# Kernel optimization log

Measured on AMD Instinct MI355X. Metric: run time of the kernel, lower is better.

The kernel has to match this reference:

```python
import jax, jax.numpy as jnp
import numpy as np

# dims
B, P, H, W = 4, 512, 32, 32
C2 = P // 2            # 256 per-branch channels
HEAD = 4
DH = C2 // HEAD        # 64 head dim
L = H * W              # 1024 tokens
DI = 2 * C2            # 512 mamba d_inner (expand=2)
N = 64                 # d_state
R = (C2 + 15) // 16    # 16 dt_rank
KC = 4                 # d_conv


def setup_inputs() -> dict:
    key = jax.random.key(0)
    ks = jax.random.split(key, 32)
    f32 = jnp.float32
    def nrm(k, shape, s=0.02):
        return jax.random.normal(k, shape, f32) * s
    inp = {}
    inp['x'] = jax.random.normal(ks[0], (B, P, H, W), f32)
    # GambaCell rel-pos + gate conv
    inp['rel_h_c'] = jax.random.normal(ks[1], (1, C2, 1, H), f32)
    inp['rel_w_c'] = jax.random.normal(ks[2], (1, C2, W, 1), f32)
    inp['gate_w'] = nrm(ks[3], (C2, C2, 3))
    inp['gate_b'] = jnp.zeros((C2,), f32)
    # Mamba params
    inp['W_in'] = nrm(ks[4], (2 * DI, C2))
    inp['conv_w'] = nrm(ks[5], (DI, KC), 0.2)
    inp['conv_b'] = jnp.zeros((DI,), f32)
    inp['W_x'] = nrm(ks[6], (R + 2 * N, DI))
    inp['W_dt'] = nrm(ks[7], (DI, R), 0.1)
    inp['b_dt'] = jnp.full((DI,), -4.0, f32)
    inp['A_log'] = jnp.broadcast_to(jnp.log(jnp.arange(1, N + 1, dtype=f32)), (DI, N)).copy()
    inp['D_p'] = jnp.ones((DI,), f32)
    inp['W_out'] = nrm(ks[8], (C2, DI))
    # MHSA params (1x1 convs -> dense)
    inp['Wq'] = nrm(ks[9], (C2, C2)); inp['bq'] = jnp.zeros((C2,), f32)
    inp['Wk'] = nrm(ks[10], (C2, C2)); inp['bk'] = jnp.zeros((C2,), f32)
    inp['Wv'] = nrm(ks[11], (C2, C2)); inp['bv'] = jnp.zeros((C2,), f32)
    inp['rel_h_m'] = jax.random.normal(ks[12], (1, HEAD, DH, 1, H), f32) * 0.02
    inp['rel_w_m'] = jax.random.normal(ks[13], (1, HEAD, DH, W, 1), f32) * 0.02
    inp['reg_qk'] = jax.random.normal(ks[14], (1, L, L), f32)
    inp['reg_v'] = jax.random.normal(ks[15], (1, DH, L), f32)
    # Gating params
    inp['Wa'] = nrm(ks[16], (P, C2)); inp['ba'] = jnp.zeros((P,), f32)
    inp['Wb'] = nrm(ks[17], (P, C2)); inp['bb'] = jnp.zeros((P,), f32)
    inp['Wg'] = nrm(ks[18], (1, P)); inp['bg'] = jnp.zeros((1,), f32)
    return inp


def _silu(t):
    return t * jax.nn.sigmoid(t)


def _conv1x1(w, b, t):  # Conv2d kernel_size=1
    return jnp.einsum('oc,bchw->bohw', w, t) + b[None, :, None, None]


def _mamba(seq, W_in, conv_w, conv_b, W_x, W_dt, b_dt, A_log, D_p, W_out):
    # seq: (B, L, C2)
    Bn = seq.shape[0]
    xz = seq @ W_in.T                       # (B,L,2*DI)
    xi, z = jnp.split(xz, 2, axis=-1)
    # causal depthwise conv1d, kernel 4, left-pad 3, trimmed to L
    xc = jnp.transpose(xi, (0, 2, 1))       # (B,DI,L)
    xp = jnp.pad(xc, ((0, 0), (0, 0), (KC - 1, 0)))
    conv = conv_b[None, :, None]
    for kk in range(KC):
        conv = conv + conv_w[None, :, kk, None] * xp[:, :, kk:kk + L]
    xs = _silu(conv).transpose(0, 2, 1)     # (B,L,DI)
    x_dbl = xs @ W_x.T                      # (B,L,R+2N)
    dt = jax.nn.softplus(x_dbl[..., :R] @ W_dt.T + b_dt)   # (B,L,DI)
    Bm = x_dbl[..., R:R + N]                # (B,L,N)
    Cm = x_dbl[..., R + N:]                 # (B,L,N)
    A = -jnp.exp(A_log)                     # (DI,N)

    def step(h, t):
        dt_t, B_t, C_t, u_t = t             # (B,DI),(B,N),(B,N),(B,DI)
        dA = jnp.exp(dt_t[..., None] * A)   # (B,DI,N)
        h = dA * h + (dt_t * u_t)[..., None] * B_t[:, None, :]
        y = jnp.sum(h * C_t[:, None, :], axis=-1)
        return h, y

    h0 = jnp.zeros((Bn, DI, N), seq.dtype)
    scan_in = (dt.transpose(1, 0, 2), Bm.transpose(1, 0, 2),
               Cm.transpose(1, 0, 2), xs.transpose(1, 0, 2))
    _, ys = jax.lax.scan(step, h0, scan_in)  # (L,B,DI)
    y = ys.transpose(1, 0, 2) + D_p * xs
    y = y * _silu(z)
    return y @ W_out.T                      # (B,L,C2)


def _forward(x, rel_h_c, rel_w_c, gate_w, gate_b, W_in, conv_w, conv_b, W_x,
             W_dt, b_dt, A_log, D_p, W_out, Wq, bq, Wk, bk, Wv, bv,
             rel_h_m, rel_w_m, reg_qk, reg_v, Wa, ba, Wb, bb, Wg, bg):
    Bn = x.shape[0]
    x1, x2 = x[:, :C2], x[:, C2:]
    # --- GambaCell branch ---
    seq = x1.reshape(Bn, C2, L).transpose(0, 2, 1)          # (B,L,C2)
    pos = (rel_h_c + rel_w_c).reshape(1, C2, L).transpose(0, 2, 1)
    seq = seq + pos
    sc = seq.transpose(0, 2, 1)                             # (B,C2,L)
    ctx = jax.nn.sigmoid(
        jax.lax.conv_general_dilated(sc, gate_w, (1,), [(1, 1)],
                                     dimension_numbers=('NCH', 'OIH', 'NCH'))
        + gate_b[None, :, None]).transpose(0, 2, 1)          # (B,L,C2)
    ym = _mamba(seq, W_in, conv_w, conv_b, W_x, W_dt, b_dt, A_log, D_p, W_out)
    # faithful to original: view (B,L,C)->(B,C,H,W) with no permute
    out1 = (ym * ctx).reshape(Bn, C2, H, W)
    # --- MHSA branch ---
    q = _conv1x1(Wq, bq, x2).reshape(Bn, HEAD, DH, L)
    k = _conv1x1(Wk, bk, x2).reshape(Bn, HEAD, DH, L)
    v = _conv1x1(Wv, bv, x2).reshape(Bn, HEAD, DH, L)
    cc = jnp.einsum('bhdi,bhdj->bhij', q, k)                # content-content
    posm = (rel_h_m + rel_w_m).reshape(HEAD, DH, L)
    cp = jnp.einsum('hdi,bhdj->bhij', posm, q)              # position^T @ q
    energy = cc + cp                                         # (B,HEAD,L,L)
    e = jnp.concatenate([energy, jnp.broadcast_to(reg_qk[None], (Bn, 1, L, L))], axis=1)
    vp = jnp.concatenate([v, jnp.broadcast_to(reg_v[None], (Bn, 1, DH, L))], axis=1)
    attn = jax.nn.softmax(e, axis=-1)
    out = jnp.einsum('bndj,bnij->bndi', vp, attn)           # v @ attn^T
    out2 = out[:, :HEAD].reshape(Bn, C2, H, W)
    # --- Gating fusion ---
    a_proj = _conv1x1(Wa, ba, out1)
    b_proj = _conv1x1(Wb, bb, out2)
    ga = jax.nn.sigmoid(_conv1x1(Wg, bg, a_proj))
    gb = jax.nn.sigmoid(_conv1x1(Wg, bg, b_proj))
    return ga * a_proj + gb * b_proj                        # (B,P,H,W)


def reference(x, rel_h_c, rel_w_c, gate_w, gate_b, W_in, conv_w, conv_b, W_x,
              W_dt, b_dt, A_log, D_p, W_out, Wq, bq, Wk, bk, Wv, bv,
              rel_h_m, rel_w_m, reg_qk, reg_v, Wa, ba, Wb, bb, Wg, bg):
    return _forward(x, rel_h_c, rel_w_c, gate_w, gate_b, W_in, conv_w, conv_b,
                    W_x, W_dt, b_dt, A_log, D_p, W_out, Wq, bq, Wk, bk, Wv, bv,
                    rel_h_m, rel_w_m, reg_qk, reg_v, Wa, ba, Wb, bb, Wg, bg)
```

## Files before the change

kernel.cpp:

```cpp
#include <hip/hip_runtime.h>
#include <math.h>

static constexpr int Bn = 4, Pp = 512, C2 = 256, HEAD = 4, DHd = 64;
static constexpr int Ll = 1024, DIi = 512, Nn = 64, Rr = 16, KCc = 4;
static constexpr int XDW = 192;

#define DEVI __device__ __forceinline__

DEVI float sigf(float x){ return 1.0f/(1.0f+__expf(-x)); }
DEVI float softplusf(float x){ return x > 20.f ? x : log1pf(__expf(x)); }

DEVI unsigned short bfh(float f){
  unsigned int u = __float_as_uint(f);
  return (unsigned short)((u + 0x7FFFu + ((u>>16)&1u)) >> 16);
}
DEVI float bff(unsigned short h){ return __uint_as_float(((unsigned int)h)<<16); }
DEVI void wsplit(float v, unsigned short* __restrict__ h, unsigned short* __restrict__ l,
                 size_t i){
  unsigned short hh = bfh(v);
  h[i] = hh; l[i] = bfh(v - bff(hh));
}

typedef __attribute__((ext_vector_type(8))) short  bf8v;
typedef __attribute__((ext_vector_type(4))) float  f4v;
typedef __attribute__((ext_vector_type(8))) unsigned short u16x8;

__global__ void k_split(const float* __restrict__ src, unsigned short* __restrict__ h,
                        unsigned short* __restrict__ l, int n){
  int i = blockIdx.x*256 + threadIdx.x;
  if (i < n) wsplit(src[i], h, l, i);
}

__global__ void k_transpose(const float* __restrict__ x, const float* __restrict__ rh,
                            const float* __restrict__ rw, float* __restrict__ seq,
                            unsigned short* __restrict__ sh, unsigned short* __restrict__ sl,
                            unsigned short* __restrict__ x2h, unsigned short* __restrict__ x2l){
  __shared__ float t[32][33];
  int b = blockIdx.z, c0 = blockIdx.y*32, l0 = blockIdx.x*32;
  for (int i = threadIdx.y; i < 32; i += 8)
    t[i][threadIdx.x] = x[((size_t)(b*Pp + c0 + i)*Ll) + l0 + threadIdx.x];
  __syncthreads();
  for (int i = threadIdx.y; i < 32; i += 8){
    int l = l0 + i, c = c0 + threadIdx.x;
    float v = t[threadIdx.x][i];
    if (c < C2){
      float pos = rh[c*32 + (l & 31)] + rw[c*32 + (l >> 5)];
      float vv = v + pos;
      size_t o = (size_t)(b*Ll + l)*C2 + c;
      seq[o] = vv;
      wsplit(vv, sh, sl, o);
    } else {
      size_t o = (size_t)(b*Ll + l)*C2 + (c - C2);
      wsplit(v, x2h, x2l, o);
    }
  }
}

__global__ void __launch_bounds__(256) k_hgemm(
    const unsigned short* __restrict__ Ahp, const unsigned short* __restrict__ Alp,
    const unsigned short* __restrict__ Bhp, const unsigned short* __restrict__ Blp,
    float* __restrict__ C, const float* __restrict__ bias,
    int M, int N, int K, int lda, int ldb, int ldc,
    long sA1, long sA2, long sB1, long sB2, long sC1, long sC2, int act)
{
  __shared__ __align__(16) unsigned short Ah[64*40], Al[64*40], Bh[64*40], Bl[64*40];
  int z = blockIdx.z;
  const unsigned short* Abh = Ahp + (size_t)((z>>2)*sA1 + (z&3)*sA2);
  const unsigned short* Abl = Alp + (size_t)((z>>2)*sA1 + (z&3)*sA2);
  const unsigned short* Bbh = Bhp + (size_t)((z>>2)*sB1 + (z&3)*sB2);
  const unsigned short* Bbl = Blp + (size_t)((z>>2)*sB1 + (z&3)*sB2);
  float* Cb = C + (size_t)((z>>2)*sC1 + (z&3)*sC2);
  int m0 = blockIdx.y*64, n0 = blockIdx.x*64;
  int t = threadIdx.x;
  int w = t >> 6, l = t & 63;
  int g = l >> 4, r = l & 15;
  int row0 = w*16;

  f4v acc[4];
  #pragma unroll
  for (int j=0;j<4;++j) acc[j] = (f4v){0.f,0.f,0.f,0.f};

  int sr = t >> 2;
  int sc = (t & 3) * 8;

  for (int k0 = 0; k0 < K; k0 += 32){
    size_t ao = (size_t)(m0+sr)*lda + k0 + sc;
    size_t bo = (size_t)(n0+sr)*ldb + k0 + sc;
    *(u16x8*)&Ah[sr*40+sc] = *(const u16x8*)&Abh[ao];
    *(u16x8*)&Al[sr*40+sc] = *(const u16x8*)&Abl[ao];
    *(u16x8*)&Bh[sr*40+sc] = *(const u16x8*)&Bbh[bo];
    *(u16x8*)&Bl[sr*40+sc] = *(const u16x8*)&Bbl[bo];
    __syncthreads();
    bf8v a_h = *(const bf8v*)&Ah[(row0+r)*40 + g*8];
    bf8v a_l = *(const bf8v*)&Al[(row0+r)*40 + g*8];
    #pragma unroll
    for (int j=0;j<4;++j){
      bf8v b_h = *(const bf8v*)&Bh[(j*16+r)*40 + g*8];
      bf8v b_l = *(const bf8v*)&Bl[(j*16+r)*40 + g*8];
      acc[j] = __builtin_amdgcn_mfma_f32_16x16x32_bf16(a_h, b_h, acc[j], 0, 0, 0);
      acc[j] = __builtin_amdgcn_mfma_f32_16x16x32_bf16(a_h, b_l, acc[j], 0, 0, 0);
      acc[j] = __builtin_amdgcn_mfma_f32_16x16x32_bf16(a_l, b_h, acc[j], 0, 0, 0);
    }
    __syncthreads();
  }
  #pragma unroll
  for (int j=0;j<4;++j){
    int n = n0 + j*16 + r;
    float bv = bias ? bias[n] : 0.f;
    #pragma unroll
    for (int q=0;q<4;++q){
      int m = m0 + row0 + g*4 + q;
      float v = acc[j][q] + bv;
      if (act == 1) v = sigf(v);
      Cb[(size_t)m*ldc + n] = v;
    }
  }
}

__global__ void __launch_bounds__(256) k_h128(
    const unsigned short* __restrict__ Ahp, const unsigned short* __restrict__ Alp,
    const unsigned short* __restrict__ Bhp, const unsigned short* __restrict__ Blp,
    float* __restrict__ C, const float* __restrict__ bias,
    int M, int N, int K, int lda, int ldb, int ldc,
    long sA1, long sA2, long sB1, long sB2, long sC1, long sC2, int act)
{
  __shared__ __align__(16) unsigned short Ah[128*40], Al[128*40], Bh[128*40], Bl[128*40];
  int z = blockIdx.z;
  const unsigned short* Abh = Ahp + (size_t)((z>>2)*sA1 + (z&3)*sA2);
  const unsigned short* Abl = Alp + (size_t)((z>>2)*sA1 + (z&3)*sA2);
  const unsigned short* Bbh = Bhp + (size_t)((z>>2)*sB1 + (z&3)*sB2);
  const unsigned short* Bbl = Blp + (size_t)((z>>2)*sB1 + (z&3)*sB2);
  float* Cb = C + (size_t)((z>>2)*sC1 + (z&3)*sC2);
  int m0 = blockIdx.y*128, n0 = blockIdx.x*128;
  int t = threadIdx.x;
  int w = t >> 6, l = t & 63;
  int g = l >> 4, r = l & 15;
  int row0 = w*32;

  f4v acc[2][8];
  #pragma unroll
  for (int i=0;i<2;++i)
    #pragma unroll
    for (int j=0;j<8;++j) acc[i][j] = (f4v){0.f,0.f,0.f,0.f};

  int sr = t >> 1;
  int sc = (t & 1) * 16;

  for (int k0 = 0; k0 < K; k0 += 32){
    size_t ao = (size_t)(m0+sr)*lda + k0 + sc;
    size_t bo = (size_t)(n0+sr)*ldb + k0 + sc;
    *(u16x8*)&Ah[sr*40+sc]   = *(const u16x8*)&Abh[ao];
    *(u16x8*)&Ah[sr*40+sc+8] = *(const u16x8*)&Abh[ao+8];
    *(u16x8*)&Al[sr*40+sc]   = *(const u16x8*)&Abl[ao];
    *(u16x8*)&Al[sr*40+sc+8] = *(const u16x8*)&Abl[ao+8];
    *(u16x8*)&Bh[sr*40+sc]   = *(const u16x8*)&Bbh[bo];
    *(u16x8*)&Bh[sr*40+sc+8] = *(const u16x8*)&Bbh[bo+8];
    *(u16x8*)&Bl[sr*40+sc]   = *(const u16x8*)&Bbl[bo];
    *(u16x8*)&Bl[sr*40+sc+8] = *(const u16x8*)&Bbl[bo+8];
    __syncthreads();
    bf8v a_h0 = *(const bf8v*)&Ah[(row0+r)*40 + g*8];
    bf8v a_l0 = *(const bf8v*)&Al[(row0+r)*40 + g*8];
    bf8v a_h1 = *(const bf8v*)&Ah[(row0+16+r)*40 + g*8];
    bf8v a_l1 = *(const bf8v*)&Al[(row0+16+r)*40 + g*8];
    #pragma unroll
    for (int j=0;j<8;++j){
      bf8v b_h = *(const bf8v*)&Bh[(j*16+r)*40 + g*8];
      bf8v b_l = *(const bf8v*)&Bl[(j*16+r)*40 + g*8];
      acc[0][j] = __builtin_amdgcn_mfma_f32_16x16x32_bf16(a_h0, b_h, acc[0][j], 0, 0, 0);
      acc[0][j] = __builtin_amdgcn_mfma_f32_16x16x32_bf16(a_h0, b_l, acc[0][j], 0, 0, 0);
      acc[0][j] = __builtin_amdgcn_mfma_f32_16x16x32_bf16(a_l0, b_h, acc[0][j], 0, 0, 0);
      acc[1][j] = __builtin_amdgcn_mfma_f32_16x16x32_bf16(a_h1, b_h, acc[1][j], 0, 0, 0);
      acc[1][j] = __builtin_amdgcn_mfma_f32_16x16x32_bf16(a_h1, b_l, acc[1][j], 0, 0, 0);
      acc[1][j] = __builtin_amdgcn_mfma_f32_16x16x32_bf16(a_l1, b_h, acc[1][j], 0, 0, 0);
    }
    __syncthreads();
  }
  #pragma unroll
  for (int i=0;i<2;++i){
    #pragma unroll
    for (int j=0;j<8;++j){
      int n = n0 + j*16 + r;
      float bv = bias ? bias[n] : 0.f;
      #pragma unroll
      for (int q=0;q<4;++q){
        int m = m0 + row0 + i*16 + g*4 + q;
        float v = acc[i][j][q] + bv;
        if (act == 1) v = sigf(v);
        Cb[(size_t)m*ldc + n] = v;
      }
    }
  }
}

__global__ void k_padwx(const float* __restrict__ W_x, unsigned short* __restrict__ h,
                        unsigned short* __restrict__ l){
  int idx = blockIdx.x*256 + threadIdx.x;
  int row = idx >> 9;
  float v = (row < 144) ? W_x[(size_t)row*512 + (idx & 511)] : 0.f;
  wsplit(v, h, l, idx);
}

__global__ void k_im2col(const float* __restrict__ seq, unsigned short* __restrict__ h,
                         unsigned short* __restrict__ l){
  int idx = blockIdx.x*256 + threadIdx.x;
  int j  = idx % 768;
  int bl = idx / 768;
  int kk = j >> 8, c = j & 255;
  int ll = bl & 1023, b = bl >> 10;
  int ls = ll + kk - 1;
  float v = 0.f;
  if (ls >= 0 && ls < Ll) v = seq[(size_t)(b*Ll + ls)*C2 + c];
  wsplit(v, h, l, idx);
}

__global__ void k_packw(const float* __restrict__ gw, unsigned short* __restrict__ h,
                        unsigned short* __restrict__ l){
  int idx = blockIdx.x*256 + threadIdx.x;
  int j = idx % 768, o = idx / 768;
  int kk = j >> 8, i = j & 255;
  wsplit(gw[(size_t)(o*256 + i)*3 + kk], h, l, idx);
}

__global__ void k_dwconv(const float* __restrict__ xz, const float* __restrict__ cw,
                         const float* __restrict__ cb, float* __restrict__ xs,
                         unsigned short* __restrict__ h, unsigned short* __restrict__ l){
  int idx = blockIdx.x*256 + threadIdx.x;
  int d = idx & 511; int bl = idx >> 9; int ll = bl & 1023; int b = bl >> 10;
  float s = cb[d];
  #pragma unroll
  for (int kk = 0; kk < 4; ++kk){
    int ls = ll - 3 + kk;
    if (ls >= 0) s = fmaf(cw[d*4+kk], xz[(size_t)(b*Ll+ls)*1024 + d], s);
  }
  float v = s * sigf(s);
  xs[idx] = v;
  wsplit(v, h, l, idx);
}

__global__ void k_pret(const float* __restrict__ xdbl, const float* __restrict__ xs,
                       const float* __restrict__ W_dt, const float* __restrict__ b_dt,
                       float* __restrict__ dtT, float* __restrict__ dtuT){
  __shared__ float X[32][17];
  __shared__ float Wd[32][17];
  __shared__ float xsb[32][33];
  int b = blockIdx.z, d0 = blockIdx.y*32, l0 = blockIdx.x*32;
  int tx = threadIdx.x, ty = threadIdx.y;
  for (int i = ty; i < 32; i += 8){
    if (tx < 16)      X[i][tx]      = xdbl[(size_t)(b*Ll + l0 + i)*XDW + tx];
    else              Wd[i][tx-16]  = W_dt[(size_t)(d0 + i)*16 + tx - 16];
    xsb[i][tx] = xs[(size_t)(b*Ll + l0 + i)*512 + d0 + tx];
  }
  __syncthreads();
  for (int dy = ty; dy < 32; dy += 8){
    int d = d0 + dy;
    float v = b_dt[d];
    #pragma unroll
    for (int r = 0; r < 16; ++r) v = fmaf(Wd[dy][r], X[tx][r], v);
    float dt = softplusf(v);
    size_t o = ((size_t)(b*512 + d))*Ll + l0 + tx;
    dtT[o]  = dt;
    dtuT[o] = dt * xsb[tx][dy];
  }
}

__global__ void __launch_bounds__(256, 1) k_scan6(
    const float* __restrict__ dtT, const float* __restrict__ dtuT,
    const float* __restrict__ xdbl, const float* __restrict__ A_log,
    float* __restrict__ yT){
  __shared__ float Bs[32*64];
  __shared__ float Cs[32*64];
  __shared__ float pb[4*32*65];
  int t = threadIdx.x;
  int w = t >> 6, lane = t & 63;
  int blk = blockIdx.x;
  int b = blk >> 7, grp = blk & 127;
  int d = grp*4 + w;
  float Ac = -__expf(A_log[d*64 + lane]);
  float h = 0.f;
  size_t base = (size_t)b*Ll;
  size_t bd   = ((size_t)(b*512 + d))*Ll;
  int jl = lane & 31;
  bool lo = lane < 32;
  float* pbw = &pb[w*2080];
  for (int c0 = 0; c0 < Ll; c0 += 32){
    float dtv = 0.f, duv = 0.f;
    if (lo){
      dtv = dtT[bd + c0 + lane];
      duv = dtuT[bd + c0 + lane];
    }
    #pragma unroll
    for (int kk = 0; kk < 8; ++kk){
      int i = t + kk*256;
      int row = i >> 6, col = i & 63;
      size_t r2 = (base + c0 + row)*XDW;
      Bs[i] = xdbl[r2 + 16 + col];
      Cs[i] = xdbl[r2 + 80 + col];
    }
    __syncthreads();
    float ev[32], gv[32];
    #pragma unroll
    for (int l = 0; l < 32; ++l){
      float sdt = __shfl(dtv, l);
      float sdu = __shfl(duv, l);
      ev[l] = __expf(sdt*Ac);
      gv[l] = sdu*Bs[l*64 + lane];
    }
    #pragma unroll
    for (int l = 0; l < 32; ++l){
      h = fmaf(ev[l], h, gv[l]);
      pbw[l*65 + lane] = h*Cs[l*64 + lane];
    }
    __syncthreads();
    {
      const float* rp = &pbw[jl*65 + (lo ? 0 : 32)];
      float s0=0.f, s1=0.f, s2=0.f, s3=0.f;
      #pragma unroll
      for (int n = 0; n < 32; n += 4){
        s0 += rp[n]; s1 += rp[n+1]; s2 += rp[n+2]; s3 += rp[n+3];
      }
      float p = (s0+s1)+(s2+s3);
      p += __shfl_xor(p, 32);
      if (lo) yT[bd + c0 + jl] = p;
    }
    __syncthreads();
  }
}

__global__ void k_ytrans(const float* __restrict__ yT, const float* __restrict__ xs,
                         const float* __restrict__ xz, const float* __restrict__ D_p,
                         unsigned short* __restrict__ h, unsigned short* __restrict__ l){
  __shared__ float t[32][33];
  int b = blockIdx.z, d0 = blockIdx.y*32, l0 = blockIdx.x*32;
  int tx = threadIdx.x, ty = threadIdx.y;
  for (int i = ty; i < 32; i += 8)
    t[i][tx] = yT[((size_t)(b*512 + d0 + i))*Ll + l0 + tx];
  __syncthreads();
  for (int i = ty; i < 32; i += 8){
    int d = d0 + tx;
    size_t bl = (size_t)b*Ll + l0 + i;
    float p  = t[tx][i];
    float u  = xs[bl*512 + d];
    float zv = xz[bl*1024 + 512 + d];
    float v = (p + D_p[d]*u) * (zv * sigf(zv));
    wsplit(v, h, l, bl*512 + d);
  }
}

__global__ void k_pack_ab(const float* __restrict__ qt, const float* __restrict__ kt,
                          const float* __restrict__ rhm, const float* __restrict__ rwm,
                          unsigned short* __restrict__ Ahp, unsigned short* __restrict__ Alp,
                          unsigned short* __restrict__ Bhp, unsigned short* __restrict__ Blp){
  int idx = blockIdx.x*256 + threadIdx.x;
  int dd = idx & 127;
  int i  = (idx >> 7) & 1023;
  int h  = (idx >> 17) & 3;
  int b  = idx >> 19;
  float av, bv;
  if (dd < 64){
    size_t q = (size_t)(b*Ll + i)*C2 + h*64 + dd;
    av = qt[q]; bv = kt[q];
  } else {
    int d = dd - 64;
    av = rhm[(h*64+d)*32 + (i & 31)] + rwm[(h*64+d)*32 + (i >> 5)];
    bv = qt[(size_t)(b*Ll + i)*C2 + h*64 + d];
  }
  wsplit(av, Ahp, Alp, idx);
  wsplit(bv, Bhp, Blp, idx);
}

__global__ void k_vtrans(const float* __restrict__ vt, unsigned short* __restrict__ h,
                         unsigned short* __restrict__ l){
  __shared__ float t[32][33];
  int b = blockIdx.z, c0 = blockIdx.y*32, j0 = blockIdx.x*32;
  for (int i = threadIdx.y; i < 32; i += 8)
    t[i][threadIdx.x] = vt[(size_t)(b*Ll + j0 + i)*C2 + c0 + threadIdx.x];
  __syncthreads();
  for (int i = threadIdx.y; i < 32; i += 8){
    size_t o = ((size_t)(b*C2 + c0 + i))*Ll + j0 + threadIdx.x;
    wsplit(t[threadIdx.x][i], h, l, o);
  }
}

__global__ void __launch_bounds__(256) k_softmax(float* __restrict__ e){
  __shared__ float red[4];
  __shared__ float red2[4];
  size_t row = blockIdx.x;
  float* p = e + row*1024;
  int t = threadIdx.x;
  float v0 = p[t], v1 = p[t+256], v2 = p[t+512], v3 = p[t+768];
  float mx = fmaxf(fmaxf(v0,v1), fmaxf(v2,v3));
  #pragma unroll
  for (int off=32; off; off>>=1) mx = fmaxf(mx, __shfl_xor(mx, off));
  if ((t&63)==0) red[t>>6] = mx;
  __syncthreads();
  mx = fmaxf(fmaxf(red[0],red[1]), fmaxf(red[2],red[3]));
  v0 = __expf(v0-mx); v1 = __expf(v1-mx); v2 = __expf(v2-mx); v3 = __expf(v3-mx);
  float s = v0+v1+v2+v3;
  #pragma unroll
  for (int off=32; off; off>>=1) s += __shfl_xor(s, off);
  if ((t&63)==0) red2[t>>6] = s;
  __syncthreads();
  s = red2[0]+red2[1]+red2[2]+red2[3];
  float inv = 1.0f/s;
  unsigned short* ph = (unsigned short*)p;
  float r0 = v0*inv, r1 = v1*inv, r2 = v2*inv, r3 = v3*inv;
  unsigned short h0 = bfh(r0), h1 = bfh(r1), h2 = bfh(r2), h3 = bfh(r3);
  ph[t]      = h0; ph[1024+t]      = bfh(r0 - bff(h0));
  ph[t+256]  = h1; ph[1024+t+256]  = bfh(r1 - bff(h1));
  ph[t+512]  = h2; ph[1024+t+512]  = bfh(r2 - bff(h2));
  ph[t+768]  = h3; ph[1024+t+768]  = bfh(r3 - bff(h3));
}

__global__ void k_mulshuf(const float* __restrict__ ym, const float* __restrict__ ctx,
                          unsigned short* __restrict__ h, unsigned short* __restrict__ l){
  __shared__ float t[32][33];
  int b = blockIdx.z >> 2, s1 = blockIdx.z & 3;
  int c0 = blockIdx.y*32, s00 = blockIdx.x*32;
  for (int i = threadIdx.y; i < 32; i += 8){
    int c = c0 + i;
    int ll = c*4 + s1;
    size_t off = ((size_t)(b*Ll + ll))*C2 + s00 + threadIdx.x;
    t[i][threadIdx.x] = ym[off] * ctx[off];
  }
  __syncthreads();
  for (int i = threadIdx.y; i < 32; i += 8){
    int s0 = s00 + i, c = c0 + threadIdx.x;
    int s = s1*256 + s0;
    wsplit(t[threadIdx.x][i], h, l, ((size_t)(b*Ll + s))*C2 + c);
  }
}

__global__ void __launch_bounds__(256) k_gates(
    const float* __restrict__ ap, const float* __restrict__ bp,
    const float* __restrict__ Wg, const float* __restrict__ bg, float* __restrict__ g){
  __shared__ float ra[4], rb[4];
  int bl = blockIdx.x; int t = threadIdx.x;
  float sa = 0.f, sb = 0.f;
  const float* a = ap + (size_t)bl*512;
  const float* bq = bp + (size_t)bl*512;
  for (int pp = t; pp < 512; pp += 256){ float w = Wg[pp]; sa = fmaf(w, a[pp], sa); sb = fmaf(w, bq[pp], sb); }
  #pragma unroll
  for (int off=32; off; off>>=1){ sa += __shfl_xor(sa,off); sb += __shfl_xor(sb,off); }
  if ((t&63)==0){ ra[t>>6]=sa; rb[t>>6]=sb; }
  __syncthreads();
  if (t==0){
    float b0 = bg[0];
    g[bl]        = sigf(ra[0]+ra[1]+ra[2]+ra[3] + b0);
    g[4096 + bl] = sigf(rb[0]+rb[1]+rb[2]+rb[3] + b0);
  }
}

__global__ void k_final(const float* __restrict__ ap, const float* __restrict__ bp,
                        const float* __restrict__ g, float* __restrict__ out){
  int bpid = blockIdx.x; int b = bpid >> 9, p = bpid & 511;
  for (int l = threadIdx.x; l < Ll; l += 256){
    int bl = b*Ll + l;
    float ga = g[bl], gb = g[4096 + bl];
    out[((size_t)(b*Pp + p) << 10) + l] =
        ga*ap[(size_t)bl*512 + p] + gb*bp[(size_t)bl*512 + p];
  }
}

typedef unsigned short us;
static inline void hgemm(hipStream_t s, const us* Ah, const us* Al, const us* Bh, const us* Bl,
                         float* C, const float* bias, int M, int N, int K,
                         int lda, int ldb, int ldc, int act){
  dim3 g(N/64, M/64, 1), blk(256);
  k_hgemm<<<g, blk, 0, s>>>(Ah,Al,Bh,Bl,C,bias,M,N,K,lda,ldb,ldc, 0,0,0,0,0,0, act);
}

extern "C" void kernel_launch(void* const* d_in, const int* in_sizes, int n_in,
                              void* d_out, int out_size, void* d_ws, size_t ws_size,
                              hipStream_t stream) {
  const float* x      = (const float*)d_in[0];
  const float* rh_c   = (const float*)d_in[1];
  const float* rw_c   = (const float*)d_in[2];
  const float* gate_w = (const float*)d_in[3];
  const float* gate_b = (const float*)d_in[4];
  const float* W_in   = (const float*)d_in[5];
  const float* conv_w = (const float*)d_in[6];
  const float* conv_b = (const float*)d_in[7];
  const float* W_x    = (const float*)d_in[8];
  const float* W_dt   = (const float*)d_in[9];
  const float* b_dt   = (const float*)d_in[10];
  const float* A_log  = (const float*)d_in[11];
  const float* D_p    = (const float*)d_in[12];
  const float* W_out  = (const float*)d_in[13];
  const float* Wq     = (const float*)d_in[14];
  const float* bq     = (const float*)d_in[15];
  const float* Wk     = (const float*)d_in[16];
  const float* bk     = (const float*)d_in[17];
  const float* Wv     = (const float*)d_in[18];
  const float* bv     = (const float*)d_in[19];
  const float* rhm    = (const float*)d_in[20];
  const float* rwm    = (const float*)d_in[21];
  const float* Wa     = (const float*)d_in[24];
  const float* ba     = (const float*)d_in[25];
  const float* Wb     = (const float*)d_in[26];
  const float* bb     = (const float*)d_in[27];
  const float* Wg     = (const float*)d_in[28];
  const float* bg     = (const float*)d_in[29];
  float* out = (float*)d_out;
  float* ws  = (float*)d_ws;

  float* seq    = ws;
  float* x2seq  = ws +  1048576;
  float* qt     = ws +  2097152;
  float* kt     = ws +  3145728;
  float* vt     = ws +  4194304;
  float* Abuf   = ws +  5242880;
  float* Bbuf   = ws +  7340032;
  float* arena  = ws +  9437184;
  float* out2   = ws + 26214400;
  float* out1   = ws + 27262976;
  float* aproj  = ws + 28311552;
  float* bproj  = ws + 30408704;
  float* gates  = ws + 32505856;
  float* W2     = ws + 32514048;
  float* A2   = arena;
  float* ctx  = arena +  3145728;
  float* xz   = arena +  4194304;
  float* xs   = arena +  8388608;
  float* xdbl = arena + 10485760;
  float* yT   = arena + 11272192;
  float* yb   = arena + 13369344;
  float* ym   = arena + 15466496;
  float* energy = arena;

  us* seqh = (us*)out1;      us* seql = seqh + 1048576;
  us* x2h  = (us*)x2seq;     us* x2l  = x2h + 1048576;
  us* eAh  = (us*)Abuf;      us* eAl  = eAh + 2097152;
  us* eBh  = (us*)Bbuf;      us* eBl  = eBh + 2097152;
  us* vTh  = (us*)aproj;     us* vTl  = vTh + 1048576;
  us* Wqh  = (us*)arena;     us* Wql  = Wqh + 65536;
  us* Wkh  = Wqh + 131072;   us* Wkl  = Wqh + 196608;
  us* Wvh  = Wqh + 262144;   us* Wvl  = Wqh + 327680;
  us* Ph   = (us*)energy;    us* Pl   = Ph + 1024;
  us* A2h  = (us*)A2;        us* A2l  = A2h + 3145728;
  us* W2h  = (us*)W2;        us* W2l  = W2h + 196608;
  us* Wm   = (us*)kt;
  us* Winh = Wm;             us* Winl = Wm + 262144;
  us* Woh  = Wm + 524288;    us* Wol  = Wm + 655360;
  us* Wah  = Wm + 786432;    us* Wal  = Wm + 917504;
  us* Wbh  = Wm + 1048576;   us* Wbl  = Wm + 1179648;
  us* Wxh  = Wm + 1310720;   us* Wxl  = Wm + 1409024;
  us* xsh  = (us*)qt;        us* xsl  = (us*)vt;
  us* ybh  = (us*)yb;        us* ybl  = ybh + 2097152;
  us* o1h  = (us*)out1;      us* o1l  = o1h + 1048576;
  us* o2h  = (us*)qt;        us* o2l  = o2h + 1048576;
  float* dtT  = Abuf;        float* dtuT = Bbuf;

  k_transpose<<<dim3(32,16,4), dim3(32,8), 0, stream>>>(x, rh_c, rw_c, seq,
                                                        seqh, seql, x2h, x2l);

  k_split<<<256, 256, 0, stream>>>(Wq, Wqh, Wql, 65536);
  k_split<<<256, 256, 0, stream>>>(Wk, Wkh, Wkl, 65536);
  k_split<<<256, 256, 0, stream>>>(Wv, Wvh, Wvl, 65536);
  hgemm(stream, x2h, x2l, Wqh, Wql, qt, bq, 4096,256,256, 256,256,256, 0);
  hgemm(stream, x2h, x2l, Wkh, Wkl, kt, bk, 4096,256,256, 256,256,256, 0);
  hgemm(stream, x2h, x2l, Wvh, Wvl, vt, bv, 4096,256,256, 256,256,256, 0);
  k_pack_ab<<<8192, 256, 0, stream>>>(qt, kt, rhm, rwm, eAh, eAl, eBh, eBl);
  k_vtrans<<<dim3(32,8,4), dim3(32,8), 0, stream>>>(vt, vTh, vTl);
  {
    dim3 g(8, 8, 16), blk(256);
    k_h128<<<g, blk, 0, stream>>>(eAh, eAl, eBh, eBl, energy, nullptr,
        1024,1024,128, 128,128,1024,
        4L*131072, 131072, 4L*131072, 131072, 4L*1048576, 1048576, 0);
  }
  k_softmax<<<16384, 256, 0, stream>>>(energy);
  {
    dim3 g(1, 16, 16), blk(256);
    k_hgemm<<<g, blk, 0, stream>>>(Ph, Pl, vTh, vTl, out2, nullptr,
        1024,64,1024, 2048,1024,256,
        8388608, 2097152, 262144, 65536, 262144, 64, 0);
  }

  k_packw<<<768, 256, 0, stream>>>(gate_w, W2h, W2l);
  k_padwx<<<384, 256, 0, stream>>>(W_x, Wxh, Wxl);
  k_split<<<1024, 256, 0, stream>>>(W_in, Winh, Winl, 262144);
  k_split<<<512, 256, 0, stream>>>(W_out, Woh, Wol, 131072);
  k_split<<<512, 256, 0, stream>>>(Wa, Wah, Wal, 131072);
  k_split<<<512, 256, 0, stream>>>(Wb, Wbh, Wbl, 131072);
  k_im2col<<<12288, 256, 0, stream>>>(seq, A2h, A2l);
  hgemm(stream, A2h, A2l, W2h, W2l, ctx, gate_b, 4096,256,768, 768,768,256, 1);
  {
    dim3 g(8, 32, 1), blk(256);
    k_h128<<<g, blk, 0, stream>>>(seqh, seql, Winh, Winl, xz, nullptr,
        4096,1024,256, 256,256,1024, 0,0,0,0,0,0, 0);
  }
  k_dwconv<<<8192, 256, 0, stream>>>(xz, conv_w, conv_b, xs, xsh, xsl);
  hgemm(stream, xsh, xsl, Wxh, Wxl, xdbl, nullptr, 4096,192,512, 512,512,XDW, 0);
  k_pret<<<dim3(32,16,4), dim3(32,8), 0, stream>>>(xdbl, xs, W_dt, b_dt, dtT, dtuT);
  k_scan6<<<512, 256, 0, stream>>>(dtT, dtuT, xdbl, A_log, yT);
  k_ytrans<<<dim3(32,16,4), dim3(32,8), 0, stream>>>(yT, xs, xz, D_p, ybh, ybl);
  hgemm(stream, ybh, ybl, Woh, Wol, ym, nullptr, 4096,256,512, 512,512,256, 0);
  k_mulshuf<<<dim3(8,8,16), dim3(32,8), 0, stream>>>(ym, ctx, o1h, o1l);

  hgemm(stream, o1h, o1l, Wah, Wal, aproj, ba, 4096,512,256, 256,256,512, 0);
  k_split<<<4096, 256, 0, stream>>>(out2, o2h, o2l, 1048576);
  hgemm(stream, o2h, o2l, Wbh, Wbl, bproj, bb, 4096,512,256, 256,256,512, 0);
  k_gates<<<4096, 256, 0, stream>>>(aproj, bproj, Wg, bg, gates);
  k_final<<<2048, 256, 0, stream>>>(aproj, bproj, gates, out);
}
```

Measured before the change: 566.6 us.

## Fuse QKV projections, batch weight splits, fuse out2 split, prefetch scan inputs

Merges the three Q/K/V GEMMs into a single N=768 GEMM with a concatenated weight and bias, and folds all weight hi/lo bf16 splitting into two batched prep kernels instead of many small launches. The attention-output GEMM now writes split bf16 hi/lo directly, which removes a separate split pass over out2. The selective-scan kernel is changed to register-prefetch the next chunk's B/C and dt values while the current chunk is processed, and its launch bounds are raised to allow two blocks per CU. The scan change increases register pressure, and the output strides of the QKV buffer change.

```diff
diff --git a/kernel.cpp b/kernel.cpp
--- a/kernel.cpp
+++ b/kernel.cpp
@@ -24,17 +24,12 @@
 typedef __attribute__((ext_vector_type(8))) short  bf8v;
 typedef __attribute__((ext_vector_type(4))) float  f4v;
 typedef __attribute__((ext_vector_type(8))) unsigned short u16x8;
-
-__global__ void k_split(const float* __restrict__ src, unsigned short* __restrict__ h,
-                        unsigned short* __restrict__ l, int n){
-  int i = blockIdx.x*256 + threadIdx.x;
-  if (i < n) wsplit(src[i], h, l, i);
-}
+typedef unsigned short us;
 
 __global__ void k_transpose(const float* __restrict__ x, const float* __restrict__ rh,
                             const float* __restrict__ rw, float* __restrict__ seq,
-                            unsigned short* __restrict__ sh, unsigned short* __restrict__ sl,
-                            unsigned short* __restrict__ x2h, unsigned short* __restrict__ x2l){
+                            us* __restrict__ sh, us* __restrict__ sl,
+                            us* __restrict__ x2h, us* __restrict__ x2l){
   __shared__ float t[32][33];
   int b = blockIdx.z, c0 = blockIdx.y*32, l0 = blockIdx.x*32;
   for (int i = threadIdx.y; i < 32; i += 8)
@@ -56,20 +51,68 @@
   }
 }
 
+__global__ void k_wprep_a(const float* __restrict__ Wq, const float* __restrict__ Wk,
+                          const float* __restrict__ Wv, const float* __restrict__ bq,
+                          const float* __restrict__ bk, const float* __restrict__ bv,
+                          us* __restrict__ wh, us* __restrict__ wl,
+                          float* __restrict__ bqkv){
+  int i = blockIdx.x*256 + threadIdx.x;
+  if (i < 196608){
+    int w = i >> 16, j = i & 65535;
+    float v = (w==0 ? Wq[j] : (w==1 ? Wk[j] : Wv[j]));
+    wsplit(v, wh, wl, i);
+  } else if (i < 197376){
+    int j = i - 196608;
+    bqkv[j] = (j < 256) ? bq[j] : (j < 512 ? bk[j-256] : bv[j-512]);
+  }
+}
+
+__global__ void k_wprep_m(const float* __restrict__ W_in, const float* __restrict__ W_out,
+                          const float* __restrict__ Wa, const float* __restrict__ Wb,
+                          const float* __restrict__ gate_w, const float* __restrict__ W_x,
+                          us* __restrict__ Winh, us* __restrict__ Winl,
+                          us* __restrict__ Woh,  us* __restrict__ Wol,
+                          us* __restrict__ Wah,  us* __restrict__ Wal,
+                          us* __restrict__ Wbh,  us* __restrict__ Wbl,
+                          us* __restrict__ W2h,  us* __restrict__ W2l,
+                          us* __restrict__ Wxh,  us* __restrict__ Wxl){
+  int i = blockIdx.x*256 + threadIdx.x;
+  if (i < 262144){ wsplit(W_in[i], Winh, Winl, i); return; }
+  i -= 262144;
+  if (i < 131072){ wsplit(W_out[i], Woh, Wol, i); return; }
+  i -= 131072;
+  if (i < 131072){ wsplit(Wa[i], Wah, Wal, i); return; }
+  i -= 131072;
+  if (i < 131072){ wsplit(Wb[i], Wbh, Wbl, i); return; }
+  i -= 131072;
+  if (i < 196608){
+    int o = i / 768, col = i % 768;
+    int kk = col >> 8, c = col & 255;
+    wsplit(gate_w[(size_t)(o*256 + c)*3 + kk], W2h, W2l, i); return;
+  }
+  i -= 196608;
+  if (i < 98304){
+    int row = i >> 9;
+    float v = (row < 144) ? W_x[(size_t)row*512 + (i & 511)] : 0.f;
+    wsplit(v, Wxh, Wxl, i);
+  }
+}
+
 __global__ void __launch_bounds__(256) k_hgemm(
-    const unsigned short* __restrict__ Ahp, const unsigned short* __restrict__ Alp,
-    const unsigned short* __restrict__ Bhp, const unsigned short* __restrict__ Blp,
+    const us* __restrict__ Ahp, const us* __restrict__ Alp,
+    const us* __restrict__ Bhp, const us* __restrict__ Blp,
     float* __restrict__ C, const float* __restrict__ bias,
     int M, int N, int K, int lda, int ldb, int ldc,
-    long sA1, long sA2, long sB1, long sB2, long sC1, long sC2, int act)
+    long sA1, long sA2, long sB1, long sB2, long sC1, long sC2, int act,
+    us* __restrict__ Chp, us* __restrict__ Clp)
 {
-  __shared__ __align__(16) unsigned short Ah[64*40], Al[64*40], Bh[64*40], Bl[64*40];
+  __shared__ __align__(16) us Ah[64*40], Al[64*40], Bh[64*40], Bl[64*40];
   int z = blockIdx.z;
-  const unsigned short* Abh = Ahp + (size_t)((z>>2)*sA1 + (z&3)*sA2);
-  const unsigned short* Abl = Alp + (size_t)((z>>2)*sA1 + (z&3)*sA2);
-  const unsigned short* Bbh = Bhp + (size_t)((z>>2)*sB1 + (z&3)*sB2);
-  const unsigned short* Bbl = Blp + (size_t)((z>>2)*sB1 + (z&3)*sB2);
-  float* Cb = C + (size_t)((z>>2)*sC1 + (z&3)*sC2);
+  const us* Abh = Ahp + (size_t)((z>>2)*sA1 + (z&3)*sA2);
+  const us* Abl = Alp + (size_t)((z>>2)*sA1 + (z&3)*sA2);
+  const us* Bbh = Bhp + (size_t)((z>>2)*sB1 + (z&3)*sB2);
+  const us* Bbl = Blp + (size_t)((z>>2)*sB1 + (z&3)*sB2);
+  size_t zco = (size_t)((z>>2)*sC1 + (z&3)*sC2);
   int m0 = blockIdx.y*64, n0 = blockIdx.x*64;
   int t = threadIdx.x;
   int w = t >> 6, l = t & 63;
@@ -112,24 +155,26 @@
       int m = m0 + row0 + g*4 + q;
       float v = acc[j][q] + bv;
       if (act == 1) v = sigf(v);
-      Cb[(size_t)m*ldc + n] = v;
+      size_t idx = zco + (size_t)m*ldc + n;
+      if (Chp) wsplit(v, Chp, Clp, idx);
+      else     C[idx] = v;
     }
   }
 }
 
 __global__ void __launch_bounds__(256) k_h128(
-    const unsigned short* __restrict__ Ahp, const unsigned short* __restrict__ Alp,
-    const unsigned short* __restrict__ Bhp, const unsigned short* __restrict__ Blp,
+    const us* __restrict__ Ahp, const us* __restrict__ Alp,
+    const us* __restrict__ Bhp, const us* __restrict__ Blp,
     float* __restrict__ C, const float* __restrict__ bias,
     int M, int N, int K, int lda, int ldb, int ldc,
     long sA1, long sA2, long sB1, long sB2, long sC1, long sC2, int act)
 {
-  __shared__ __align__(16) unsigned short Ah[128*40], Al[128*40], Bh[128*40], Bl[128*40];
+  __shared__ __align__(16) us Ah[128*40], Al[128*40], Bh[128*40], Bl[128*40];
   int z = blockIdx.z;
-  const unsigned short* Abh = Ahp + (size_t)((z>>2)*sA1 + (z&3)*sA2);
-  const unsigned short* Abl = Alp + (size_t)((z>>2)*sA1 + (z&3)*sA2);
-  const unsigned short* Bbh = Bhp + (size_t)((z>>2)*sB1 + (z&3)*sB2);
-  const unsigned short* Bbl = Blp + (size_t)((z>>2)*sB1 + (z&3)*sB2);
+  const us* Abh = Ahp + (size_t)((z>>2)*sA1 + (z&3)*sA2);
+  const us* Abl = Alp + (size_t)((z>>2)*sA1 + (z&3)*sA2);
+  const us* Bbh = Bhp + (size_t)((z>>2)*sB1 + (z&3)*sB2);
+  const us* Bbl = Blp + (size_t)((z>>2)*sB1 + (z&3)*sB2);
   float* Cb = C + (size_t)((z>>2)*sC1 + (z&3)*sC2);
   int m0 = blockIdx.y*128, n0 = blockIdx.x*128;
   int t = threadIdx.x;
@@ -192,16 +237,8 @@
   }
 }
 
-__global__ void k_padwx(const float* __restrict__ W_x, unsigned short* __restrict__ h,
-                        unsigned short* __restrict__ l){
-  int idx = blockIdx.x*256 + threadIdx.x;
-  int row = idx >> 9;
-  float v = (row < 144) ? W_x[(size_t)row*512 + (idx & 511)] : 0.f;
-  wsplit(v, h, l, idx);
-}
-
-__global__ void k_im2col(const float* __restrict__ seq, unsigned short* __restrict__ h,
-                         unsigned short* __restrict__ l){
+__global__ void k_im2col(const float* __restrict__ seq, us* __restrict__ h,
+                         us* __restrict__ l){
   int idx = blockIdx.x*256 + threadIdx.x;
   int j  = idx % 768;
   int bl = idx / 768;
@@ -213,17 +250,9 @@
   wsplit(v, h, l, idx);
 }
 
-__global__ void k_packw(const float* __restrict__ gw, unsigned short* __restrict__ h,
-                        unsigned short* __restrict__ l){
-  int idx = blockIdx.x*256 + threadIdx.x;
-  int j = idx % 768, o = idx / 768;
-  int kk = j >> 8, i = j & 255;
-  wsplit(gw[(size_t)(o*256 + i)*3 + kk], h, l, idx);
-}
-
 __global__ void k_dwconv(const float* __restrict__ xz, const float* __restrict__ cw,
                          const float* __restrict__ cb, float* __restrict__ xs,
-                         unsigned short* __restrict__ h, unsigned short* __restrict__ l){
+                         us* __restrict__ h, us* __restrict__ l){
   int idx = blockIdx.x*256 + threadIdx.x;
   int d = idx & 511; int bl = idx >> 9; int ll = bl & 1023; int b = bl >> 10;
   float s = cb[d];
@@ -263,7 +292,7 @@
   }
 }
 
-__global__ void __launch_bounds__(256, 1) k_scan6(
+__global__ void __launch_bounds__(256, 2) k_scan7(
     const float* __restrict__ dtT, const float* __restrict__ dtuT,
     const float* __restrict__ xdbl, const float* __restrict__ A_log,
     float* __restrict__ yT){
@@ -282,26 +311,42 @@
   int jl = lane & 31;
   bool lo = lane < 32;
   float* pbw = &pb[w*2080];
+  float rB[8], rC[8];
+  float dtv = 0.f, duv = 0.f;
+  #pragma unroll
+  for (int kk = 0; kk < 8; ++kk){
+    int i = t + kk*256;
+    int row = i >> 6, col = i & 63;
+    size_t r2 = (base + row)*XDW;
+    rB[kk] = xdbl[r2 + 16 + col];
+    rC[kk] = xdbl[r2 + 80 + col];
+  }
+  if (lo){ dtv = dtT[bd + lane]; duv = dtuT[bd + lane]; }
   for (int c0 = 0; c0 < Ll; c0 += 32){
-    float dtv = 0.f, duv = 0.f;
-    if (lo){
-      dtv = dtT[bd + c0 + lane];
-      duv = dtuT[bd + c0 + lane];
-    }
     #pragma unroll
     for (int kk = 0; kk < 8; ++kk){
       int i = t + kk*256;
-      int row = i >> 6, col = i & 63;
-      size_t r2 = (base + c0 + row)*XDW;
-      Bs[i] = xdbl[r2 + 16 + col];
-      Cs[i] = xdbl[r2 + 80 + col];
-    }
+      Bs[i] = rB[kk]; Cs[i] = rC[kk];
+    }
+    float dtc = dtv, duc = duv;
     __syncthreads();
+    int c1 = c0 + 32;
+    if (c1 < Ll){
+      #pragma unroll
+      for (int kk = 0; kk < 8; ++kk){
+        int i = t + kk*256;
+        int row = i >> 6, col = i & 63;
+        size_t r2 = (base + c1 + row)*XDW;
+        rB[kk] = xdbl[r2 + 16 + col];
+        rC[kk] = xdbl[r2 + 80 + col];
+      }
+      if (lo){ dtv = dtT[bd + c1 + lane]; duv = dtuT[bd + c1 + lane]; }
+    }
     float ev[32], gv[32];
     #pragma unroll
     for (int l = 0; l < 32; ++l){
-      float sdt = __shfl(dtv, l);
-      float sdu = __shfl(duv, l);
+      float sdt = __shfl(dtc, l);
+      float sdu = __shfl(duc, l);
       ev[l] = __expf(sdt*Ac);
       gv[l] = sdu*Bs[l*64 + lane];
     }
@@ -328,7 +373,7 @@
 
 __global__ void k_ytrans(const float* __restrict__ yT, const float* __restrict__ xs,
                          const float* __restrict__ xz, const float* __restrict__ D_p,
-                         unsigned short* __restrict__ h, unsigned short* __restrict__ l){
+                         us* __restrict__ h, us* __restrict__ l){
   __shared__ float t[32][33];
   int b = blockIdx.z, d0 = blockIdx.y*32, l0 = blockIdx.x*32;
   int tx = threadIdx.x, ty = threadIdx.y;
@@ -346,10 +391,10 @@
   }
 }
 
-__global__ void k_pack_ab(const float* __restrict__ qt, const float* __restrict__ kt,
+__global__ void k_pack_ab(const float* __restrict__ qkv,
                           const float* __restrict__ rhm, const float* __restrict__ rwm,
-                          unsigned short* __restrict__ Ahp, unsigned short* __restrict__ Alp,
-                          unsigned short* __restrict__ Bhp, unsigned short* __restrict__ Blp){
+                          us* __restrict__ Ahp, us* __restrict__ Alp,
+                          us* __restrict__ Bhp, us* __restrict__ Blp){
   int idx = blockIdx.x*256 + threadIdx.x;
   int dd = idx & 127;
   int i  = (idx >> 7) & 1023;
@@ -357,23 +402,23 @@
   int b  = idx >> 19;
   float av, bv;
   if (dd < 64){
-    size_t q = (size_t)(b*Ll + i)*C2 + h*64 + dd;
-    av = qt[q]; bv = kt[q];
+    size_t q = (size_t)(b*Ll + i)*768 + h*64 + dd;
+    av = qkv[q]; bv = qkv[q + 256];
   } else {
     int d = dd - 64;
     av = rhm[(h*64+d)*32 + (i & 31)] + rwm[(h*64+d)*32 + (i >> 5)];
-    bv = qt[(size_t)(b*Ll + i)*C2 + h*64 + d];
+    bv = qkv[(size_t)(b*Ll + i)*768 + h*64 + d];
   }
   wsplit(av, Ahp, Alp, idx);
   wsplit(bv, Bhp, Blp, idx);
 }
 
-__global__ void k_vtrans(const float* __restrict__ vt, unsigned short* __restrict__ h,
-                         unsigned short* __restrict__ l){
+__global__ void k_vtrans(const float* __restrict__ qkv, us* __restrict__ h,
+                         us* __restrict__ l){
   __shared__ float t[32][33];
   int b = blockIdx.z, c0 = blockIdx.y*32, j0 = blockIdx.x*32;
   for (int i = threadIdx.y; i < 32; i += 8)
-    t[i][threadIdx.x] = vt[(size_t)(b*Ll + j0 + i)*C2 + c0 + threadIdx.x];
+    t[i][threadIdx.x] = qkv[(size_t)(b*Ll + j0 + i)*768 + 512 + c0 + threadIdx.x];
   __syncthreads();
   for (int i = threadIdx.y; i < 32; i += 8){
     size_t o = ((size_t)(b*C2 + c0 + i))*Ll + j0 + threadIdx.x;
@@ -402,9 +447,9 @@
   __syncthreads();
   s = red2[0]+red2[1]+red2[2]+red2[3];
   float inv = 1.0f/s;
-  unsigned short* ph = (unsigned short*)p;
+  us* ph = (us*)p;
   float r0 = v0*inv, r1 = v1*inv, r2 = v2*inv, r3 = v3*inv;
-  unsigned short h0 = bfh(r0), h1 = bfh(r1), h2 = bfh(r2), h3 = bfh(r3);
+  us h0 = bfh(r0), h1 = bfh(r1), h2 = bfh(r2), h3 = bfh(r3);
   ph[t]      = h0; ph[1024+t]      = bfh(r0 - bff(h0));
   ph[t+256]  = h1; ph[1024+t+256]  = bfh(r1 - bff(h1));
   ph[t+512]  = h2; ph[1024+t+512]  = bfh(r2 - bff(h2));
@@ -412,7 +457,7 @@
 }
 
 __global__ void k_mulshuf(const float* __restrict__ ym, const float* __restrict__ ctx,
-                          unsigned short* __restrict__ h, unsigned short* __restrict__ l){
+                          us* __restrict__ h, us* __restrict__ l){
   __shared__ float t[32][33];
   int b = blockIdx.z >> 2, s1 = blockIdx.z & 3;
   int c0 = blockIdx.y*32, s00 = blockIdx.x*32;
@@ -461,12 +506,12 @@
   }
 }
 
-typedef unsigned short us;
 static inline void hgemm(hipStream_t s, const us* Ah, const us* Al, const us* Bh, const us* Bl,
                          float* C, const float* bias, int M, int N, int K,
                          int lda, int ldb, int ldc, int act){
   dim3 g(N/64, M/64, 1), blk(256);
-  k_hgemm<<<g, blk, 0, s>>>(Ah,Al,Bh,Bl,C,bias,M,N,K,lda,ldb,ldc, 0,0,0,0,0,0, act);
+  k_hgemm<<<g, blk, 0, s>>>(Ah,Al,Bh,Bl,C,bias,M,N,K,lda,ldb,ldc, 0,0,0,0,0,0, act,
+                            nullptr, nullptr);
 }
 
 extern "C" void kernel_launch(void* const* d_in, const int* in_sizes, int n_in,
@@ -505,13 +550,11 @@
 
   float* seq    = ws;
   float* x2seq  = ws +  1048576;
-  float* qt     = ws +  2097152;
-  float* kt     = ws +  3145728;
-  float* vt     = ws +  4194304;
+  float* qkv    = ws +  2097152;
   float* Abuf   = ws +  5242880;
   float* Bbuf   = ws +  7340032;
   float* arena  = ws +  9437184;
-  float* out2   = ws + 26214400;
+  float* out2s  = ws + 26214400;
   float* out1   = ws + 27262976;
   float* aproj  = ws + 28311552;
   float* bproj  = ws + 30408704;
@@ -532,35 +575,30 @@
   us* eAh  = (us*)Abuf;      us* eAl  = eAh + 2097152;
   us* eBh  = (us*)Bbuf;      us* eBl  = eBh + 2097152;
   us* vTh  = (us*)aproj;     us* vTl  = vTh + 1048576;
-  us* Wqh  = (us*)arena;     us* Wql  = Wqh + 65536;
-  us* Wkh  = Wqh + 131072;   us* Wkl  = Wqh + 196608;
-  us* Wvh  = Wqh + 262144;   us* Wvl  = Wqh + 327680;
+  us* wqkvh = (us*)arena;    us* wqkvl = wqkvh + 196608;
+  float* bqkv = arena + 196608;
   us* Ph   = (us*)energy;    us* Pl   = Ph + 1024;
   us* A2h  = (us*)A2;        us* A2l  = A2h + 3145728;
   us* W2h  = (us*)W2;        us* W2l  = W2h + 196608;
-  us* Wm   = (us*)kt;
+  us* Wm   = (us*)(qkv + 1048576);
   us* Winh = Wm;             us* Winl = Wm + 262144;
   us* Woh  = Wm + 524288;    us* Wol  = Wm + 655360;
   us* Wah  = Wm + 786432;    us* Wal  = Wm + 917504;
   us* Wbh  = Wm + 1048576;   us* Wbl  = Wm + 1179648;
   us* Wxh  = Wm + 1310720;   us* Wxl  = Wm + 1409024;
-  us* xsh  = (us*)qt;        us* xsl  = (us*)vt;
+  us* xsh  = (us*)qkv;       us* xsl  = (us*)(qkv + 2097152);
   us* ybh  = (us*)yb;        us* ybl  = ybh + 2097152;
   us* o1h  = (us*)out1;      us* o1l  = o1h + 1048576;
-  us* o2h  = (us*)qt;        us* o2l  = o2h + 1048576;
+  us* o2h  = (us*)out2s;     us* o2l  = o2h + 1048576;
   float* dtT  = Abuf;        float* dtuT = Bbuf;
 
   k_transpose<<<dim3(32,16,4), dim3(32,8), 0, stream>>>(x, rh_c, rw_c, seq,
                                                         seqh, seql, x2h, x2l);
 
-  k_split<<<256, 256, 0, stream>>>(Wq, Wqh, Wql, 65536);
-  k_split<<<256, 256, 0, stream>>>(Wk, Wkh, Wkl, 65536);
-  k_split<<<256, 256, 0, stream>>>(Wv, Wvh, Wvl, 65536);
-  hgemm(stream, x2h, x2l, Wqh, Wql, qt, bq, 4096,256,256, 256,256,256, 0);
-  hgemm(stream, x2h, x2l, Wkh, Wkl, kt, bk, 4096,256,256, 256,256,256, 0);
-  hgemm(stream, x2h, x2l, Wvh, Wvl, vt, bv, 4096,256,256, 256,256,256, 0);
-  k_pack_ab<<<8192, 256, 0, stream>>>(qt, kt, rhm, rwm, eAh, eAl, eBh, eBl);
-  k_vtrans<<<dim3(32,8,4), dim3(32,8), 0, stream>>>(vt, vTh, vTl);
+  k_wprep_a<<<772, 256, 0, stream>>>(Wq, Wk, Wv, bq, bk, bv, wqkvh, wqkvl, bqkv);
+  hgemm(stream, x2h, x2l, wqkvh, wqkvl, qkv, bqkv, 4096,768,256, 256,256,768, 0);
+  k_pack_ab<<<8192, 256, 0, stream>>>(qkv, rhm, rwm, eAh, eAl, eBh, eBl);
+  k_vtrans<<<dim3(32,8,4), dim3(32,8), 0, stream>>>(qkv, vTh, vTl);
   {
     dim3 g(8, 8, 16), blk(256);
     k_h128<<<g, blk, 0, stream>>>(eAh, eAl, eBh, eBl, energy, nullptr,
@@ -570,17 +608,13 @@
   k_softmax<<<16384, 256, 0, stream>>>(energy);
   {
     dim3 g(1, 16, 16), blk(256);
-    k_hgemm<<<g, blk, 0, stream>>>(Ph, Pl, vTh, vTl, out2, nullptr,
+    k_hgemm<<<g, blk, 0, stream>>>(Ph, Pl, vTh, vTl, nullptr, nullptr,
         1024,64,1024, 2048,1024,256,
-        8388608, 2097152, 262144, 65536, 262144, 64, 0);
-  }
-
-  k_packw<<<768, 256, 0, stream>>>(gate_w, W2h, W2l);
-  k_padwx<<<384, 256, 0, stream>>>(W_x, Wxh, Wxl);
-  k_split<<<1024, 256, 0, stream>>>(W_in, Winh, Winl, 262144);
-  k_split<<<512, 256, 0, stream>>>(W_out, Woh, Wol, 131072);
-  k_split<<<512, 256, 0, stream>>>(Wa, Wah, Wal, 131072);
-  k_split<<<512, 256, 0, stream>>>(Wb, Wbh, Wbl, 131072);
+        8388608, 2097152, 262144, 65536, 262144, 64, 0, o2h, o2l);
+  }
+
+  k_wprep_m<<<3713, 256, 0, stream>>>(W_in, W_out, Wa, Wb, gate_w, W_x,
+      Winh, Winl, Woh, Wol, Wah, Wal, Wbh, Wbl, W2h, W2l, Wxh, Wxl);
   k_im2col<<<12288, 256, 0, stream>>>(seq, A2h, A2l);
   hgemm(stream, A2h, A2l, W2h, W2l, ctx, gate_b, 4096,256,768, 768,768,256, 1);
   {
@@ -591,13 +625,12 @@
   k_dwconv<<<8192, 256, 0, stream>>>(xz, conv_w, conv_b, xs, xsh, xsl);
   hgemm(stream, xsh, xsl, Wxh, Wxl, xdbl, nullptr, 4096,192,512, 512,512,XDW, 0);
   k_pret<<<dim3(32,16,4), dim3(32,8), 0, stream>>>(xdbl, xs, W_dt, b_dt, dtT, dtuT);
-  k_scan6<<<512, 256, 0, stream>>>(dtT, dtuT, xdbl, A_log, yT);
+  k_scan7<<<512, 256, 0, stream>>>(dtT, dtuT, xdbl, A_log, yT);
   k_ytrans<<<dim3(32,16,4), dim3(32,8), 0, stream>>>(yT, xs, xz, D_p, ybh, ybl);
   hgemm(stream, ybh, ybl, Woh, Wol, ym, nullptr, 4096,256,512, 512,512,256, 0);
   k_mulshuf<<<dim3(8,8,16), dim3(32,8), 0, stream>>>(ym, ctx, o1h, o1l);
 
   hgemm(stream, o1h, o1l, Wah, Wal, aproj, ba, 4096,512,256, 256,256,512, 0);
-  k_split<<<4096, 256, 0, stream>>>(out2, o2h, o2l, 1048576);
   hgemm(stream, o2h, o2l, Wbh, Wbl, bproj, bb, 4096,512,256, 256,256,512, 0);
   k_gates<<<4096, 256, 0, stream>>>(aproj, bproj, Wg, bg, gates);
   k_final<<<2048, 256, 0, stream>>>(aproj, bproj, gates, out);
```

Result: faster. 534.3 us (-5.7%).
